# Kernel tuning notes

Measured on AMD Instinct MI355X. Metric: run time of the kernel, lower is better.

## Reference

```python
import jax, jax.numpy as jnp
import numpy as np

TGT_LEN = 1024
MEM_LEN = 1024
SAME_LENGTH = True
D_MODEL = 2048
BATCH = 4


def _make_ft_real(tgt_len: int, mem_len: int, same_length: bool) -> jnp.ndarray:
    """Build the banded Fourier mixing matrix. Since the module's input x is real
    and only .real of the output is returned, Re(FT @ x) == Re(FT) @ x, so we
    precompute only the real part (this also matches the kernel-headroom note:
    the imaginary output is never used)."""
    qlen = tgt_len
    klen = tgt_len + mem_len
    flen = klen - qlen + 1
    m = np.outer(np.arange(qlen), np.arange(flen))
    ft = np.exp(2j * np.pi * m / flen) / np.sqrt(flen)  # [qlen, flen] complex
    ft = np.pad(ft, ((0, 0), (klen - flen, 0)))          # left-pad to [qlen, klen]
    for i in range(qlen):  # setup-time numpy loop over fixed qlen rows (not traced)
        ft[i] = np.roll(ft[i], -(qlen - i - 1))
    ft = np.tril(ft, klen - qlen)
    if same_length:
        ft = np.triu(ft, 0)
    return jnp.asarray(ft.real.astype(np.float32))


_FT_REAL = _make_ft_real(TGT_LEN, MEM_LEN, SAME_LENGTH)  # [tgt_len, tgt_len+mem_len]


def setup_inputs() -> dict:
    key = jax.random.key(0)
    k1, k2 = jax.random.split(key)
    klen = TGT_LEN + MEM_LEN
    x = jax.random.normal(k1, (BATCH, klen, D_MODEL), dtype=jnp.float32)
    p = jax.random.normal(k2, (BATCH, klen, D_MODEL), dtype=jnp.float32)
    return {"x": x, "p": p, "qlen": TGT_LEN, "add_position": 1}


def reference(x, p, qlen, add_position):
    # Dropout is identity in eval mode (deterministic reference).
    if add_position:
        x = x + p
    klen = x.shape[1]
    ft = _FT_REAL[-qlen:, -klen:]                    # [qlen, klen]
    scale = np.float32(1.0 / np.sqrt(klen))
    # Banded token-mixing matmul; real part only (x is real).
    out = jnp.einsum("lm,bmd->bld", ft, x) * scale   # [B, qlen, D]
    return out
```

## Files before the change

### kernel.cpp

```cpp
#include <hip/hip_runtime.h>
#include <hip/hip_bf16.h>
#include <cstdint>

#define QLEN   1024
#define KLEN   2048
#define DMODEL 2048
#define BATCH  4
#define FLEN   (KLEN - QLEN + 1)

typedef __bf16 bf16x8 __attribute__((ext_vector_type(8)));
typedef __bf16 bf16x4 __attribute__((ext_vector_type(4)));
typedef float  f32x4  __attribute__((ext_vector_type(4)));

__device__ __bf16 g_ft[(size_t)QLEN * KLEN];
__device__ __bf16 g_yt[(size_t)BATCH * DMODEL * KLEN];

typedef __attribute__((address_space(1))) void gvoid;
typedef __attribute__((address_space(3))) void svoid;

__device__ __forceinline__ void async_load16(const void* g, void* lds) {
  gvoid* gp = (gvoid*)(uintptr_t)g;
  svoid* sp = (svoid*)(uint32_t)(uintptr_t)lds;
  __builtin_amdgcn_global_load_lds(gp, sp, 16, 0, 0);
}

__global__ void gen_ft_kernel() {
  const int u  = blockIdx.x * 256 + threadIdx.x;
  const int l  = u >> 8;
  const int m0 = (u & 255) * 8;
  const int j0 = m0 - l;
  bf16x8 o = {};
  if (j0 + 7 >= 0 && j0 < FLEN) {
    const float w     = 6.283185307179586f / (float)FLEN;
    const float scale = 1.0f / sqrtf((float)FLEN * (float)KLEN);
#pragma unroll
    for (int i = 0; i < 8; ++i) {
      const int j = j0 + i;
      float v = 0.0f;
      if (j >= 0 && j < FLEN) {
        const int r = (l * j) % FLEN;
        v = cosf((float)r * w) * scale;
      }
      o[i] = (__bf16)v;
    }
  }
  *(bf16x8*)(g_ft + (size_t)u * 8) = o;
}

__global__ __launch_bounds__(256) void gen_yt_kernel(const float* __restrict__ x,
                                                     const float* __restrict__ p,
                                                     const int* __restrict__ addp) {
  __shared__ __align__(16) float xt[64 * 64];
  __shared__ __align__(16) float pt[64 * 64];
  const int b  = blockIdx.z;
  const int m0 = blockIdx.x * 64;
  const int d0 = blockIdx.y * 64;
  const int t  = threadIdx.x;
  const int lane = t & 63;
  const int wave = t >> 6;
  const float addf = (*addp) ? 1.0f : 0.0f;
  const size_t base = (size_t)b * KLEN * DMODEL;

#pragma unroll
  for (int q = 0; q < 4; ++q) {
    const int cb = q * 256 + wave * 64;
    const int fc = cb + lane;
    const int m  = fc >> 4;
    const int cl = fc & 15;
    const int gc = cl ^ ((m >> 3) & 7);
    async_load16(x + base + (size_t)(m0 + m) * DMODEL + d0 + gc * 4, xt + cb * 4);
  }
#pragma unroll
  for (int q = 0; q < 4; ++q) {
    const int cb = q * 256 + wave * 64;
    const int fc = cb + lane;
    const int m  = fc >> 4;
    const int cl = fc & 15;
    const int gc = cl ^ ((m >> 3) & 7);
    async_load16(p + base + (size_t)(m0 + m) * DMODEL + d0 + gc * 4, pt + cb * 4);
  }
  __syncthreads();

#pragma unroll
  for (int s = 0; s < 2; ++s) {
    const int u  = t + 256 * s;
    const int d  = u >> 3;
    const int mc = u & 7;
    bf16x8 o;
#pragma unroll
    for (int i = 0; i < 8; ++i) {
      const int idx = (mc * 8 + i) * 64 + 4 * ((d >> 2) ^ mc) + (d & 3);
      o[i] = (__bf16)(xt[idx] + addf * pt[idx]);
    }
    *(bf16x8*)(g_yt + base + (size_t)(d0 + d) * KLEN + (m0 + mc * 8)) = o;
  }
}

#define BM 128
#define BN 128
#define BK 64

__global__ __launch_bounds__(256) void gemm_kernel(float* __restrict__ out) {
  __shared__ __align__(16) __bf16 As[BM * BK];
  __shared__ __align__(16) __bf16 Bs[BN * BK];
  const int bn = blockIdx.x, bm = blockIdx.y, b = blockIdx.z;
  const int l0 = bm * BM, d0 = bn * BN;
  const int tid  = threadIdx.x;
  const int lane = tid & 63;
  const int wave = tid >> 6;
  const int wr = wave >> 1, wc = wave & 1;
  const int col = lane & 15, quad = lane >> 4;

  f32x4 acc[4][4] = {};

  const int t0 = l0 >> 6;
  const int t1 = (l0 + BM - 1 + FLEN - 1) >> 6;
  const __bf16* ftp = g_ft;
  const __bf16* ytp = g_yt + (size_t)b * DMODEL * KLEN;

  for (int t = t0; t <= t1; ++t) {
    const int k0 = t * BK;
#pragma unroll
    for (int s = 0; s < 4; ++s) {
      const int cb  = wave * 256 + s * 64;
      const int lc  = cb + lane;
      const int row = lc >> 3;
      const int gc8 = (lc & 7) ^ (row & 7);
      async_load16(ftp + (size_t)(l0 + row) * KLEN + k0 + gc8 * 8, As + cb * 8);
    }
#pragma unroll
    for (int s = 0; s < 4; ++s) {
      const int cb  = wave * 256 + s * 64;
      const int lc  = cb + lane;
      const int row = lc >> 3;
      const int gc8 = (lc & 7) ^ (row & 7);
      async_load16(ytp + (size_t)(d0 + row) * KLEN + k0 + gc8 * 8, Bs + cb * 8);
    }
    __syncthreads();

#pragma unroll
    for (int kk = 0; kk < 2; ++kk) {
      bf16x8 af[4], bq[4];
      const int c8 = kk * 4 + quad;
#pragma unroll
      for (int ti = 0; ti < 4; ++ti) {
        const int r = wr * 64 + ti * 16 + col;
        af[ti] = *(const bf16x8*)(As + (size_t)((r << 3) + (c8 ^ (r & 7))) * 8);
      }
#pragma unroll
      for (int tj = 0; tj < 4; ++tj) {
        const int r = wc * 64 + tj * 16 + col;
        bq[tj] = *(const bf16x8*)(Bs + (size_t)((r << 3) + (c8 ^ (r & 7))) * 8);
      }
#pragma unroll
      for (int ti = 0; ti < 4; ++ti)
#pragma unroll
        for (int tj = 0; tj < 4; ++tj)
          acc[ti][tj] = __builtin_amdgcn_mfma_f32_16x16x32_bf16(af[ti], bq[tj], acc[ti][tj], 0, 0, 0);
    }
    __syncthreads();
  }

#pragma unroll
  for (int ti = 0; ti < 4; ++ti) {
    const int l = l0 + wr * 64 + ti * 16 + quad * 4;
#pragma unroll
    for (int tj = 0; tj < 4; ++tj) {
      const int d = d0 + wc * 64 + tj * 16 + col;
      float* op = out + (size_t)b * QLEN * DMODEL + (size_t)l * DMODEL + d;
#pragma unroll
      for (int r2 = 0; r2 < 4; ++r2) op[(size_t)r2 * DMODEL] = acc[ti][tj][r2];
    }
  }
}

extern "C" void kernel_launch(void* const* d_in, const int* in_sizes, int n_in,
                              void* d_out, int out_size, void* d_ws, size_t ws_size,
                              hipStream_t stream) {
  const float* x   = (const float*)d_in[0];
  const float* p   = (const float*)d_in[1];
  const int* addp  = (const int*)d_in[3];
  float* out = (float*)d_out;

  gen_ft_kernel<<<dim3((QLEN * KLEN / 8) / 256), dim3(256), 0, stream>>>();
  gen_yt_kernel<<<dim3(KLEN / 64, DMODEL / 64, BATCH), dim3(256), 0, stream>>>(x, p, addp);
  gemm_kernel<<<dim3(DMODEL / BN, QLEN / BM, BATCH), dim3(256), 0, stream>>>(out);
}
```

Before: 206.2 us.

## Merge prep kernels and store Y in k-chunked layout to skip transpose

Replaces the separate FT-generation and LDS-transposing Y kernels with a single grid-stride prep kernel. It writes x+p as bf16 in a layout of 8-element k chunks by d, so no shared-memory transpose is needed and loads stay coalesced. The GEMM's B-tile load and LDS read indexing are changed to match this layout and drop the XOR swizzle. This saves one launch and the transpose traffic. The unswizzled B reads may cause LDS bank conflicts, and the grid-stride loop mixes memory-bound and trig-heavy units in one kernel.

Result: faster. 195.5 us (-5.2%).

```diff
diff --git a/kernel.cpp b/kernel.cpp
--- a/kernel.cpp
+++ b/kernel.cpp
@@ -9,11 +9,10 @@
 #define FLEN   (KLEN - QLEN + 1)
 
 typedef __bf16 bf16x8 __attribute__((ext_vector_type(8)));
-typedef __bf16 bf16x4 __attribute__((ext_vector_type(4)));
 typedef float  f32x4  __attribute__((ext_vector_type(4)));
 
-__device__ __bf16 g_ft[(size_t)QLEN * KLEN];
-__device__ __bf16 g_yt[(size_t)BATCH * DMODEL * KLEN];
+__device__ __align__(16) __bf16 g_ft[(size_t)QLEN * KLEN];
+__device__ __align__(16) __bf16 g_yt[(size_t)BATCH * DMODEL * KLEN];
 
 typedef __attribute__((address_space(1))) void gvoid;
 typedef __attribute__((address_space(3))) void svoid;
@@ -24,75 +23,59 @@
   __builtin_amdgcn_global_load_lds(gp, sp, 16, 0, 0);
 }
 
-__global__ void gen_ft_kernel() {
-  const int u  = blockIdx.x * 256 + threadIdx.x;
-  const int l  = u >> 8;
-  const int m0 = (u & 255) * 8;
-  const int j0 = m0 - l;
-  bf16x8 o = {};
-  if (j0 + 7 >= 0 && j0 < FLEN) {
-    const float w     = 6.283185307179586f / (float)FLEN;
-    const float scale = 1.0f / sqrtf((float)FLEN * (float)KLEN);
+#define YT_UNITS (BATCH * (KLEN / 8) * (DMODEL / 64))
+#define FT_UNITS ((QLEN * KLEN) / 512)
+
+__global__ __launch_bounds__(256) void prep_kernel(const float* __restrict__ x,
+                                                   const float* __restrict__ p,
+                                                   const int* __restrict__ addp) {
+  const int lane  = threadIdx.x & 63;
+  const int gw    = (blockIdx.x * 256 + threadIdx.x) >> 6;
+  const int nw    = gridDim.x * 4;
+  const int doadd = *addp;
+
+  for (int u = gw; u < YT_UNITS + FT_UNITS; u += nw) {
+    if (u < YT_UNITS) {
+      const int b  = u >> 13;
+      const int r5 = u & 8191;
+      const int mt = r5 >> 5;
+      const int db = r5 & 31;
+      const int d  = db * 64 + lane;
+      const float* xp = x + ((size_t)b * KLEN + mt * 8) * DMODEL + d;
+      float v[8];
 #pragma unroll
-    for (int i = 0; i < 8; ++i) {
-      const int j = j0 + i;
-      float v = 0.0f;
-      if (j >= 0 && j < FLEN) {
-        const int r = (l * j) % FLEN;
-        v = cosf((float)r * w) * scale;
+      for (int i = 0; i < 8; ++i) v[i] = xp[(size_t)i * DMODEL];
+      if (doadd) {
+        const float* pp = p + ((size_t)b * KLEN + mt * 8) * DMODEL + d;
+#pragma unroll
+        for (int i = 0; i < 8; ++i) v[i] += pp[(size_t)i * DMODEL];
       }
-      o[i] = (__bf16)v;
+      bf16x8 o;
+#pragma unroll
+      for (int i = 0; i < 8; ++i) o[i] = (__bf16)v[i];
+      *(bf16x8*)(g_yt + ((size_t)b * (KLEN / 8) * DMODEL + (size_t)mt * DMODEL + d) * 8) = o;
+    } else {
+      const int uu = (u - YT_UNITS) * 64 + lane;
+      const int l  = uu >> 8;
+      const int m0 = (uu & 255) * 8;
+      const int j0 = m0 - l;
+      bf16x8 o = {};
+      if (j0 + 7 >= 0 && j0 < FLEN) {
+        const float w     = 6.283185307179586f / (float)FLEN;
+        const float scale = 1.0f / sqrtf((float)FLEN * (float)KLEN);
+#pragma unroll
+        for (int i = 0; i < 8; ++i) {
+          const int j = j0 + i;
+          float vv = 0.0f;
+          if (j >= 0 && j < FLEN) {
+            const int rr = (l * j) % FLEN;
+            vv = cosf((float)rr * w) * scale;
+          }
+          o[i] = (__bf16)vv;
+        }
+      }
+      *(bf16x8*)(g_ft + (size_t)uu * 8) = o;
     }
-  }
-  *(bf16x8*)(g_ft + (size_t)u * 8) = o;
-}
-
-__global__ __launch_bounds__(256) void gen_yt_kernel(const float* __restrict__ x,
-                                                     const float* __restrict__ p,
-                                                     const int* __restrict__ addp) {
-  __shared__ __align__(16) float xt[64 * 64];
-  __shared__ __align__(16) float pt[64 * 64];
-  const int b  = blockIdx.z;
-  const int m0 = blockIdx.x * 64;
-  const int d0 = blockIdx.y * 64;
-  const int t  = threadIdx.x;
-  const int lane = t & 63;
-  const int wave = t >> 6;
-  const float addf = (*addp) ? 1.0f : 0.0f;
-  const size_t base = (size_t)b * KLEN * DMODEL;
-
-#pragma unroll
-  for (int q = 0; q < 4; ++q) {
-    const int cb = q * 256 + wave * 64;
-    const int fc = cb + lane;
-    const int m  = fc >> 4;
-    const int cl = fc & 15;
-    const int gc = cl ^ ((m >> 3) & 7);
-    async_load16(x + base + (size_t)(m0 + m) * DMODEL + d0 + gc * 4, xt + cb * 4);
-  }
-#pragma unroll
-  for (int q = 0; q < 4; ++q) {
-    const int cb = q * 256 + wave * 64;
-    const int fc = cb + lane;
-    const int m  = fc >> 4;
-    const int cl = fc & 15;
-    const int gc = cl ^ ((m >> 3) & 7);
-    async_load16(p + base + (size_t)(m0 + m) * DMODEL + d0 + gc * 4, pt + cb * 4);
-  }
-  __syncthreads();
-
-#pragma unroll
-  for (int s = 0; s < 2; ++s) {
-    const int u  = t + 256 * s;
-    const int d  = u >> 3;
-    const int mc = u & 7;
-    bf16x8 o;
-#pragma unroll
-    for (int i = 0; i < 8; ++i) {
-      const int idx = (mc * 8 + i) * 64 + 4 * ((d >> 2) ^ mc) + (d & 3);
-      o[i] = (__bf16)(xt[idx] + addf * pt[idx]);
-    }
-    *(bf16x8*)(g_yt + base + (size_t)(d0 + d) * KLEN + (m0 + mc * 8)) = o;
   }
 }
 
@@ -130,11 +113,10 @@
     }
 #pragma unroll
     for (int s = 0; s < 4; ++s) {
-      const int cb  = wave * 256 + s * 64;
-      const int lc  = cb + lane;
-      const int row = lc >> 3;
-      const int gc8 = (lc & 7) ^ (row & 7);
-      async_load16(ytp + (size_t)(d0 + row) * KLEN + k0 + gc8 * 8, Bs + cb * 8);
+      const int idx = wave * 256 + s * 64 + lane;
+      const int c   = idx >> 7;
+      const int dd  = idx & 127;
+      async_load16(ytp + ((size_t)(t * 8 + c) * DMODEL + (d0 + dd)) * 8, Bs + (size_t)idx * 8);
     }
     __syncthreads();
 
@@ -150,7 +132,7 @@
 #pragma unroll
       for (int tj = 0; tj < 4; ++tj) {
         const int r = wc * 64 + tj * 16 + col;
-        bq[tj] = *(const bf16x8*)(Bs + (size_t)((r << 3) + (c8 ^ (r & 7))) * 8);
+        bq[tj] = *(const bf16x8*)(Bs + (size_t)((c8 << 7) + r) * 8);
       }
 #pragma unroll
       for (int ti = 0; ti < 4; ++ti)
@@ -182,7 +164,6 @@
   const int* addp  = (const int*)d_in[3];
   float* out = (float*)d_out;
 
-  gen_ft_kernel<<<dim3((QLEN * KLEN / 8) / 256), dim3(256), 0, stream>>>();
-  gen_yt_kernel<<<dim3(KLEN / 64, DMODEL / 64, BATCH), dim3(256), 0, stream>>>(x, p, addp);
+  prep_kernel<<<dim3(2048), dim3(256), 0, stream>>>(x, p, addp);
   gemm_kernel<<<dim3(DMODEL / BN, QLEN / BM, BATCH), dim3(256), 0, stream>>>(out);
 }
```
